# Kernel tuning notes

Measured on AMD Instinct MI355X. Metric: run time of the kernel, lower is better.

Reference implementation:

```python
import jax, jax.numpy as jnp
import numpy as np

N = 50000      # nodes
E = 400000     # edges (before self-loops)
F_IN = 256     # input_dim
HID = 64       # hidden_dim (per-head)
H = 4          # heads
OUT = 16       # output_dim
NEG_SLOPE = 0.2


def _gat_layer(x, W, a_src, a_dst, b, src, dst):
    # x: [N, Fin], W: [Fin, H*HID], a_src/a_dst: [H, HID], b: [H*HID]
    n = x.shape[0]
    h = (x @ W).reshape(n, H, HID)                        # [N,H,D]
    es = jnp.einsum('nhd,hd->nh', h, a_src)               # [N,H]
    ed = jnp.einsum('nhd,hd->nh', h, a_dst)               # [N,H]
    e = jax.nn.leaky_relu(es[src] + ed[dst], NEG_SLOPE)   # [E,H]
    m = jax.ops.segment_max(e, dst, num_segments=n)       # [N,H] segment softmax (stable)
    m = jnp.where(jnp.isfinite(m), m, 0.0)
    p = jnp.exp(e - m[dst])
    s = jax.ops.segment_sum(p, dst, num_segments=n)
    alpha = p / (s[dst] + 1e-16)                          # [E,H]
    out = jax.ops.segment_sum(h[src] * alpha[:, :, None], dst, num_segments=n)  # [N,H,D]
    return out.reshape(n, H * HID) + b


def setup_inputs() -> dict:
    key = jax.random.key(0)
    ks = jax.random.split(key, 24)
    lin = lambda k, i, o: (jax.random.normal(k, (i, o), jnp.float32) / np.sqrt(i)).astype(jnp.float32)
    att = lambda k: (jax.random.normal(k, (H, HID), jnp.float32) * 0.1).astype(jnp.float32)
    FH = H * HID  # 256
    inp = {
        'x': jax.random.normal(ks[0], (N, F_IN), jnp.float32),
        'edge_index': jax.random.randint(ks[1], (2, E), 0, N, dtype=jnp.int64),
        'W1': lin(ks[2], F_IN, FH), 'a1_src': att(ks[3]), 'a1_dst': att(ks[4]), 'b1': jnp.zeros((FH,), jnp.float32),
        'W2': lin(ks[5], FH, FH),   'a2_src': att(ks[6]), 'a2_dst': att(ks[7]), 'b2': jnp.zeros((FH,), jnp.float32),
        'W3': lin(ks[8], FH, FH),   'a3_src': att(ks[9]), 'a3_dst': att(ks[10]), 'b3': jnp.zeros((FH,), jnp.float32),
        'pW1': lin(ks[11], FH, HID), 'pb1': jnp.zeros((HID,), jnp.float32),
        'pW2': lin(ks[12], HID, HID), 'pb2': jnp.zeros((HID,), jnp.float32),
        'cW1': lin(ks[13], FH, HID), 'cb1': jnp.zeros((HID,), jnp.float32),
        'cW2': lin(ks[14], HID, OUT), 'cb2': jnp.zeros((OUT,), jnp.float32),
    }
    return inp


def reference(x, edge_index, W1, a1_src, a1_dst, b1, W2, a2_src, a2_dst, b2,
              W3, a3_src, a3_dst, b3, pW1, pb1, pW2, pb2, cW1, cb1, cW2, cb2):
    n = x.shape[0]
    loop = jnp.arange(n, dtype=edge_index.dtype)          # PyG GATConv adds self-loops
    src = jnp.concatenate([edge_index[0], loop])
    dst = jnp.concatenate([edge_index[1], loop])
    h = jax.nn.elu(_gat_layer(x, W1, a1_src, a1_dst, b1, src, dst))
    h = jax.nn.elu(_gat_layer(h, W2, a2_src, a2_dst, b2, src, dst))
    h = _gat_layer(h, W3, a3_src, a3_dst, b3, src, dst)   # [N, 256]
    logits = jax.nn.relu(h @ cW1 + cb1) @ cW2 + cb2       # classifier (dropout inactive, eval)
    proj = jax.nn.relu(h @ pW1 + pb1) @ pW2 + pb2         # projection head
    return jax.nn.log_softmax(logits, axis=1), proj
```

## Files before the change

### kernel.cpp

```cpp
#include <hip/hip_runtime.h>
#include <hip/hip_bf16.h>

#define NN 50000
#define EE 400000
#define TE (EE + NN)
#define SCAN_B ((NN + 255) / 256)

typedef float f4 __attribute__((ext_vector_type(4)));
typedef __bf16 b8 __attribute__((ext_vector_type(8)));
typedef unsigned short us8 __attribute__((ext_vector_type(8)));

__device__ __forceinline__ float b2f(unsigned short u) {
    union { unsigned int i; float f; } c; c.i = ((unsigned int)u) << 16; return c.f;
}
__device__ __forceinline__ unsigned short f2b(float x) {
    union { unsigned int i; float f; } c; c.f = x;
    unsigned int i = c.i;
    return (unsigned short)((i + 0x7FFFu + ((i >> 16) & 1u)) >> 16);
}
__device__ __forceinline__ int clampi(int v, int lo, int hi) {
    return v < lo ? lo : (v > hi ? hi : v);
}

#define PO_WT    0
#define PO_ATT   196608
#define PO_BT    198912
#define PO_BIAS  231680
#define PO_PW2   231808
#define PO_PB2   235904
#define PO_CW2   235968
#define PO_CB2   236992
#define PO_BT2   237008
#define PO_BIAS2 253392
#define PO_TOTAL 253520

__global__ void detect_kernel(const int* __restrict__ ei, const unsigned int* __restrict__ xw,
                              int* __restrict__ flag) {
    int lane = threadIdx.x;
    int bad = (lane < 16 && ei[2 * lane + 1] != 0) ? 1 : 0;
    int cnt = 0;
#pragma unroll
    for (int k = 0; k < 4; k++) {
        int i = lane + k * 64;
        unsigned short lo = (unsigned short)(xw[i] & 0xFFFFu);
        int e = (lo >> 7) & 0xFF;
        if (e >= 120 && e <= 132) cnt++;
    }
    unsigned long long anybad = __ballot(bad != 0);
#pragma unroll
    for (int off = 1; off < 64; off <<= 1) cnt += __shfl_xor(cnt, off, 64);
    if (lane == 0) {
        flag[0] = (anybad == 0ULL) ? 1 : 0;
        flag[1] = (cnt >= 128) ? 1 : 0;
    }
}

__global__ __launch_bounds__(256) void convx_kernel(const void* __restrict__ src,
                                                    unsigned short* __restrict__ dst,
                                                    const int* __restrict__ flag) {
    int i = blockIdx.x * 256 + threadIdx.x;
    if (i >= NN * 256 / 4) return;
    if (flag[1]) {
        ((ushort4*)dst)[i] = ((const ushort4*)src)[i];
    } else {
        float4 v = ((const float4*)src)[i];
        ushort4 o; o.x = f2b(v.x); o.y = f2b(v.y); o.z = f2b(v.z); o.w = f2b(v.w);
        ((ushort4*)dst)[i] = o;
    }
}

__device__ __forceinline__ float ldf(const void* p, int i, int bf) {
    return bf ? b2f(((const unsigned short*)p)[i]) : ((const float*)p)[i];
}
__global__ __launch_bounds__(256) void prep_kernel(
    const void* W1, const void* W2, const void* W3,
    const void* as1, const void* ad1, const void* b1,
    const void* as2, const void* ad2, const void* b2,
    const void* as3, const void* ad3, const void* b3,
    const void* pW1, const void* pb1, const void* pW2, const void* pb2,
    const void* cW1, const void* cb1, const void* cW2, const void* cb2,
    unsigned short* __restrict__ P, const int* __restrict__ flag) {
    int idx = blockIdx.x * 256 + threadIdx.x;
    if (idx >= PO_TOTAL) return;
    int bf = flag[1];
    float v;
    if (idx < PO_ATT) {
        int l = idx / 65536, r = idx % 65536;
        int n = r >> 8, k = r & 255;
        const void* W = (l == 0) ? W1 : (l == 1) ? W2 : W3;
        v = ldf(W, k * 256 + n, bf);
    } else if (idx < PO_BT) {
        int r = idx - PO_ATT;
        int l = r / 768, w = r % 768, which = w >> 8, j = w & 255;
        const void* s;
        if (which == 0) s = (l == 0) ? as1 : (l == 1) ? as2 : as3;
        else if (which == 1) s = (l == 0) ? ad1 : (l == 1) ? ad2 : ad3;
        else s = (l == 0) ? b1 : (l == 1) ? b2 : b3;
        v = ldf(s, j, bf);
    } else if (idx < PO_BIAS) {
        int r3 = idx - PO_BT;
        int r = r3 >> 8, k = r3 & 255;
        v = (r < 64) ? ldf(cW1, k * 64 + r, bf) : ldf(pW1, k * 64 + (r - 64), bf);
    } else if (idx < PO_PW2) {
        int r = idx - PO_BIAS;
        v = (r < 64) ? ldf(cb1, r, bf) : ldf(pb1, r - 64, bf);
    } else if (idx < PO_PB2) {
        v = ldf(pW2, idx - PO_PW2, bf);
    } else if (idx < PO_CW2) {
        v = ldf(pb2, idx - PO_PB2, bf);
    } else if (idx < PO_CB2) {
        v = ldf(cW2, idx - PO_CW2, bf);
    } else if (idx < PO_BT2) {
        v = ldf(cb2, idx - PO_CB2, bf);
    } else if (idx < PO_BIAS2) {
        int r2 = idx - PO_BT2;
        int r = r2 >> 7, k = r2 & 127;
        if (r < 16) v = (k < 64) ? ldf(cW2, k * 16 + r, bf) : 0.f;
        else if (r < 80) v = (k >= 64) ? ldf(pW2, (k - 64) * 64 + (r - 16), bf) : 0.f;
        else v = 0.f;
    } else {
        int r = idx - PO_BIAS2;
        v = (r < 16) ? ldf(cb2, r, bf) : (r < 80 ? ldf(pb2, r - 16, bf) : 0.f);
    }
    P[idx] = f2b(v);
}

__device__ __forceinline__ void edge_decode(const int* __restrict__ ei, int mode64, int e,
                                            int& src, int& dst) {
    if (e < EE) {
        if (mode64) { src = ei[2 * e]; dst = ei[2 * EE + 2 * e]; }
        else        { src = ei[e];     dst = ei[EE + e]; }
        src = clampi(src, 0, NN - 1);
        dst = clampi(dst, 0, NN - 1);
    } else {
        src = dst = e - EE;
    }
}

__global__ void deg_kernel(const int* __restrict__ ei, const int* __restrict__ flag,
                           int* __restrict__ deg) {
    int e = blockIdx.x * 256 + threadIdx.x;
    if (e >= TE) return;
    int src, dst;
    edge_decode(ei, flag[0], e, src, dst);
    atomicAdd(&deg[dst], 1);
}

__global__ __launch_bounds__(256) void scanA_kernel(const int* __restrict__ deg,
                                                    int* __restrict__ offs, int* __restrict__ bsum) {
    __shared__ int s[256];
    int t = threadIdx.x, i = blockIdx.x * 256 + t;
    int v = (i < NN) ? deg[i] : 0;
    s[t] = v;
    __syncthreads();
    for (int off = 1; off < 256; off <<= 1) {
        int x = (t >= off) ? s[t - off] : 0;
        __syncthreads();
        s[t] += x;
        __syncthreads();
    }
    if (i < NN) offs[i] = s[t] - v;
    if (t == 255) bsum[blockIdx.x] = s[255];
}
__global__ __launch_bounds__(256) void scanB_kernel(int* __restrict__ bsum) {
    __shared__ int s[256];
    int t = threadIdx.x;
    int v = (t < SCAN_B) ? bsum[t] : 0;
    s[t] = v;
    __syncthreads();
    for (int off = 1; off < 256; off <<= 1) {
        int x = (t >= off) ? s[t - off] : 0;
        __syncthreads();
        s[t] += x;
        __syncthreads();
    }
    if (t < SCAN_B) bsum[t] = s[t] - v;
}
__global__ __launch_bounds__(256) void scanC_kernel(int* __restrict__ offs,
                                                    const int* __restrict__ bsum) {
    int t = threadIdx.x, i = blockIdx.x * 256 + t;
    if (i < NN) offs[i] += bsum[blockIdx.x];
    if (i == 0) offs[NN] = TE;
}

__global__ void scatter_kernel(const int* __restrict__ ei, const int* __restrict__ flag,
                               const int* __restrict__ offs,
                               int* __restrict__ cursor, int* __restrict__ srcs,
                               int* __restrict__ dsts) {
    int e = blockIdx.x * 256 + threadIdx.x;
    if (e >= TE) return;
    int src, dst;
    edge_decode(ei, flag[0], e, src, dst);
    int pos = atomicAdd(&cursor[dst], 1);
    int slot = offs[dst] + pos;
    if (slot >= 0 && slot < TE) { srcs[slot] = src; dsts[slot] = dst; }
}

__device__ __forceinline__ void async_ld16(const unsigned short* g, unsigned short* l) {
    __builtin_amdgcn_global_load_lds(
        (const __attribute__((address_space(1))) unsigned int*)g,
        (__attribute__((address_space(3))) unsigned int*)l, 16, 0, 0);
}

__global__ __launch_bounds__(256) void gemm_bt_kernel(
    const unsigned short* __restrict__ A, const unsigned short* __restrict__ Bt,
    unsigned short* __restrict__ C, int M, int Nc, int K,
    const unsigned short* __restrict__ bias, int relu, int outf32, int final,
    const unsigned short* __restrict__ asrc, const unsigned short* __restrict__ adst,
    float* __restrict__ es, float* __restrict__ ed) {
    __shared__ unsigned short As[128 * 32];
    __shared__ unsigned short Bs[128 * 32];
    int tid = threadIdx.x;
    int lane = tid & 63;
    int wave = tid >> 6;
    int wr = wave >> 1, wc = wave & 1;
    int m0 = blockIdx.x * 128;
    int n0 = blockIdx.y * 128;
    f4 acc[4][4];
#pragma unroll
    for (int i = 0; i < 4; i++)
#pragma unroll
        for (int j = 0; j < 4; j++) acc[i][j] = (f4){0.f, 0.f, 0.f, 0.f};

    int rin = lane >> 2;
    int qsl = lane & 3;
    int qg  = qsl ^ ((rin >> 1) & 3);
    int rsel = lane & 15;
    int q16 = lane >> 4;
    int slotq = q16 ^ ((rsel >> 1) & 3);

    for (int kt = 0; kt < K; kt += 32) {
#pragma unroll
        for (int t = 0; t < 4; t++) {
            int seg = wave * 4 + t;
            if (seg < 8) {
                int r = seg * 16 + rin;
                int gm = m0 + r;
                if (gm < M)
                    async_ld16(A + (size_t)gm * K + kt + qg * 8, &As[seg * 512]);
            } else {
                int r = (seg - 8) * 16 + rin;
                int gn = n0 + r;
                async_ld16(Bt + (size_t)gn * K + kt + qg * 8, &Bs[(seg - 8) * 512]);
            }
        }
        __syncthreads();
        b8 af[4], bfv[4];
#pragma unroll
        for (int i = 0; i < 4; i++) {
            af[i]  = *(const b8*)(&As[(wr * 64 + i * 16 + rsel) * 32 + slotq * 8]);
            bfv[i] = *(const b8*)(&Bs[(wc * 64 + i * 16 + rsel) * 32 + slotq * 8]);
        }
#pragma unroll
        for (int i = 0; i < 4; i++)
#pragma unroll
            for (int j = 0; j < 4; j++)
                acc[i][j] = __builtin_amdgcn_mfma_f32_16x16x32_bf16(af[i], bfv[j], acc[i][j], 0, 0, 0);
        __syncthreads();
    }
    int cl = lane & 15, rq = lane >> 4;
    if (es) {
        int head = blockIdx.y * 2 + wc;
        float asv[4], adv[4];
#pragma unroll
        for (int j = 0; j < 4; j++) {
            asv[j] = b2f(asrc[head * 64 + j * 16 + cl]);
            adv[j] = b2f(adst[head * 64 + j * 16 + cl]);
        }
#pragma unroll
        for (int i = 0; i < 4; i++) {
            float pes[4], ped[4];
#pragma unroll
            for (int r = 0; r < 4; r++) {
                float se = 0.f, de = 0.f;
#pragma unroll
                for (int j = 0; j < 4; j++) {
                    se += acc[i][j][r] * asv[j];
                    de += acc[i][j][r] * adv[j];
                }
                pes[r] = se; ped[r] = de;
            }
#pragma unroll
            for (int off = 1; off < 16; off <<= 1) {
#pragma unroll
                for (int r = 0; r < 4; r++) {
                    pes[r] += __shfl_xor(pes[r], off, 64);
                    ped[r] += __shfl_xor(ped[r], off, 64);
                }
            }
            if (cl == 0) {
#pragma unroll
                for (int r = 0; r < 4; r++) {
                    int row = m0 + wr * 64 + i * 16 + rq * 4 + r;
                    if (row < M) {
                        es[(size_t)row * 4 + head] = pes[r];
                        ed[(size_t)row * 4 + head] = ped[r];
                    }
                }
            }
        }
    }
    if (final) {
        float* flog  = (float*)C;
        float* fproj = flog + (size_t)M * 16;
#pragma unroll
        for (int i = 0; i < 4; i++) {
#pragma unroll
            for (int r = 0; r < 4; r++) {
                int row = m0 + wr * 64 + i * 16 + rq * 4 + r;
                if (row >= M) continue;
                if (wc == 0) {
                    float lv = acc[i][0][r] + b2f(bias[cl]);
                    float mx = lv;
#pragma unroll
                    for (int off = 1; off < 16; off <<= 1) mx = fmaxf(mx, __shfl_xor(mx, off, 64));
                    float se = __expf(lv - mx);
#pragma unroll
                    for (int off = 1; off < 16; off <<= 1) se += __shfl_xor(se, off, 64);
                    flog[(size_t)row * 16 + cl] = lv - mx - __logf(se);
#pragma unroll
                    for (int j = 1; j < 4; j++) {
                        float pv = acc[i][j][r] + b2f(bias[j * 16 + cl]);
                        fproj[(size_t)row * 64 + j * 16 + cl - 16] = pv;
                    }
                } else {
                    float pv = acc[i][0][r] + b2f(bias[64 + cl]);
                    fproj[(size_t)row * 64 + 48 + cl] = pv;
                }
            }
        }
        return;
    }
#pragma unroll
    for (int j = 0; j < 4; j++) {
        int col = n0 + wc * 64 + j * 16 + cl;
        float bv = bias ? b2f(bias[col]) : 0.0f;
#pragma unroll
        for (int i = 0; i < 4; i++) {
#pragma unroll
            for (int r = 0; r < 4; r++) {
                int row = m0 + wr * 64 + i * 16 + rq * 4 + r;
                if (row < M) {
                    float v = acc[i][j][r] + bv;
                    if (relu) v = fmaxf(v, 0.0f);
                    if (outf32) ((float*)C)[(size_t)row * Nc + col] = v;
                    else C[(size_t)row * Nc + col] = f2b(v);
                }
            }
        }
    }
}

__global__ __launch_bounds__(256) void wexp_kernel(
    const float* __restrict__ es, const float* __restrict__ ed,
    const int* __restrict__ srcs, const int* __restrict__ dsts,
    float* __restrict__ wbuf) {
    int j = blockIdx.x * 256 + threadIdx.x;
    if (j >= TE) return;
    int s = srcs[j], d = dsts[j];
    float4 a = ((const float4*)es)[s];
    float4 b = ((const float4*)ed)[d];
    float v0 = a.x + b.x, v1 = a.y + b.y, v2 = a.z + b.z, v3 = a.w + b.w;
    v0 = v0 > 0.f ? v0 : 0.2f * v0; v1 = v1 > 0.f ? v1 : 0.2f * v1;
    v2 = v2 > 0.f ? v2 : 0.2f * v2; v3 = v3 > 0.f ? v3 : 0.2f * v3;
    ((float4*)wbuf)[j] = make_float4(__expf(v0), __expf(v1), __expf(v2), __expf(v3));
}

__global__ __launch_bounds__(256) void aggr_kernel(
    const unsigned short* __restrict__ H, const float* __restrict__ wbuf,
    const int* __restrict__ offs, const int* __restrict__ srcs,
    const unsigned short* __restrict__ bias, unsigned short* __restrict__ out, int N, int elu) {
    int gw = (blockIdx.x * 256 + threadIdx.x) >> 6;
    int lane = threadIdx.x & 63;
    if (gw >= N) return;
    int half = lane >> 5;
    int lh = lane & 31;
    int ch = lh << 3;
    int head = lh >> 3;
    int j0 = offs[gw];
    int j1 = offs[gw + 1];
    float a0 = 0.f, a1 = 0.f, a2 = 0.f, a3 = 0.f;
    float a4 = 0.f, a5 = 0.f, a6 = 0.f, a7 = 0.f;
    float sw = 0.f;
    int nfull = (j1 - j0) & ~3;
    int jb = j0 + half * 2;
    for (int t = 0; t < nfull; t += 4) {
        int sA = srcs[jb + t];
        int sB = srcs[jb + t + 1];
        float wA = wbuf[(size_t)(jb + t) * 4 + head];
        float wB = wbuf[(size_t)(jb + t + 1) * 4 + head];
        us8 hA = *(const us8*)(H + (size_t)sA * 256 + ch);
        us8 hB = *(const us8*)(H + (size_t)sB * 256 + ch);
        sw += wA + wB;
        a0 += wA * b2f(hA[0]) + wB * b2f(hB[0]);
        a1 += wA * b2f(hA[1]) + wB * b2f(hB[1]);
        a2 += wA * b2f(hA[2]) + wB * b2f(hB[2]);
        a3 += wA * b2f(hA[3]) + wB * b2f(hB[3]);
        a4 += wA * b2f(hA[4]) + wB * b2f(hB[4]);
        a5 += wA * b2f(hA[5]) + wB * b2f(hB[5]);
        a6 += wA * b2f(hA[6]) + wB * b2f(hB[6]);
        a7 += wA * b2f(hA[7]) + wB * b2f(hB[7]);
    }
    for (int j = j0 + nfull + half; j < j1; j += 2) {
        int sA = srcs[j];
        float wA = wbuf[(size_t)j * 4 + head];
        us8 hA = *(const us8*)(H + (size_t)sA * 256 + ch);
        sw += wA;
        a0 += wA * b2f(hA[0]); a1 += wA * b2f(hA[1]);
        a2 += wA * b2f(hA[2]); a3 += wA * b2f(hA[3]);
        a4 += wA * b2f(hA[4]); a5 += wA * b2f(hA[5]);
        a6 += wA * b2f(hA[6]); a7 += wA * b2f(hA[7]);
    }
    sw += __shfl_xor(sw, 32, 64);
    a0 += __shfl_xor(a0, 32, 64); a1 += __shfl_xor(a1, 32, 64);
    a2 += __shfl_xor(a2, 32, 64); a3 += __shfl_xor(a3, 32, 64);
    a4 += __shfl_xor(a4, 32, 64); a5 += __shfl_xor(a5, 32, 64);
    a6 += __shfl_xor(a6, 32, 64); a7 += __shfl_xor(a7, 32, 64);
    if (half == 0) {
        float rs = 1.f / (sw + 1e-16f);
        us8 bv = *(const us8*)(bias + ch);
        float r0 = a0 * rs + b2f(bv[0]), r1 = a1 * rs + b2f(bv[1]);
        float r2 = a2 * rs + b2f(bv[2]), r3 = a3 * rs + b2f(bv[3]);
        float r4 = a4 * rs + b2f(bv[4]), r5 = a5 * rs + b2f(bv[5]);
        float r6 = a6 * rs + b2f(bv[6]), r7 = a7 * rs + b2f(bv[7]);
        if (elu) {
            r0 = r0 > 0.f ? r0 : __expf(r0) - 1.f;
            r1 = r1 > 0.f ? r1 : __expf(r1) - 1.f;
            r2 = r2 > 0.f ? r2 : __expf(r2) - 1.f;
            r3 = r3 > 0.f ? r3 : __expf(r3) - 1.f;
            r4 = r4 > 0.f ? r4 : __expf(r4) - 1.f;
            r5 = r5 > 0.f ? r5 : __expf(r5) - 1.f;
            r6 = r6 > 0.f ? r6 : __expf(r6) - 1.f;
            r7 = r7 > 0.f ? r7 : __expf(r7) - 1.f;
        }
        us8 o;
        o[0] = f2b(r0); o[1] = f2b(r1); o[2] = f2b(r2); o[3] = f2b(r3);
        o[4] = f2b(r4); o[5] = f2b(r5); o[6] = f2b(r6); o[7] = f2b(r7);
        *(us8*)(out + (size_t)gw * 256 + ch) = o;
    }
}

extern "C" void kernel_launch(void* const* d_in, const int* in_sizes, int n_in,
                              void* d_out, int out_size, void* d_ws, size_t ws_size,
                              hipStream_t stream) {
    (void)in_sizes; (void)n_in; (void)out_size; (void)ws_size;
    const int* ei = (const int*)d_in[1];

    char* p = (char*)d_ws;
    auto take = [&](size_t bytes) -> void* {
        void* r = (void*)p;
        p += (bytes + 255) & ~(size_t)255;
        return r;
    };
    int* flag   = (int*)take(256);
    int* deg    = (int*)take((size_t)NN * 4);
    int* cursor = (int*)take((size_t)NN * 4);
    int* offs   = (int*)take((size_t)(NN + 1) * 4);
    int* bsum   = (int*)take(256 * 4);
    int* srcs   = (int*)take((size_t)TE * 4);
    int* dsts   = (int*)take((size_t)TE * 4);
    float* es   = (float*)take((size_t)NN * 16);
    float* ed   = (float*)take((size_t)NN * 16);
    float* wbuf = (float*)take((size_t)TE * 16);
    unsigned short* bufH = (unsigned short*)take((size_t)NN * 256 * 2);
    unsigned short* buf1 = (unsigned short*)take((size_t)NN * 256 * 2);
    unsigned short* buf2 = (unsigned short*)take((size_t)NN * 256 * 2);
    unsigned short* P    = (unsigned short*)take((size_t)PO_TOTAL * 2);
    unsigned short* xb = buf2;
    unsigned short* tbuf = bufH;

    detect_kernel<<<1, 64, 0, stream>>>(ei, (const unsigned int*)d_in[0], flag);
    convx_kernel<<<NN * 256 / 4 / 256, 256, 0, stream>>>(d_in[0], xb, flag);
    prep_kernel<<<(PO_TOTAL + 255) / 256, 256, 0, stream>>>(
        d_in[2], d_in[6], d_in[10],
        d_in[3], d_in[4], d_in[5],
        d_in[7], d_in[8], d_in[9],
        d_in[11], d_in[12], d_in[13],
        d_in[14], d_in[15], d_in[16], d_in[17],
        d_in[18], d_in[19], d_in[20], d_in[21],
        P, flag);

    hipMemsetAsync(deg, 0, (size_t)NN * 4, stream);
    hipMemsetAsync(cursor, 0, (size_t)NN * 4, stream);
    deg_kernel<<<(TE + 255) / 256, 256, 0, stream>>>(ei, flag, deg);
    scanA_kernel<<<SCAN_B, 256, 0, stream>>>(deg, offs, bsum);
    scanB_kernel<<<1, 256, 0, stream>>>(bsum);
    scanC_kernel<<<SCAN_B, 256, 0, stream>>>(offs, bsum);
    scatter_kernel<<<(TE + 255) / 256, 256, 0, stream>>>(ei, flag, offs, cursor, srcs, dsts);

    const unsigned short* X = xb;
    unsigned short* outbuf[3] = {buf1, buf2, buf1};
    for (int l = 0; l < 3; l++) {
        const unsigned short* Wt  = P + PO_WT + l * 65536;
        const unsigned short* asr = P + PO_ATT + l * 768;
        const unsigned short* adr = P + PO_ATT + l * 768 + 256;
        const unsigned short* bcb = P + PO_ATT + l * 768 + 512;
        gemm_bt_kernel<<<dim3((NN + 127) / 128, 2), 256, 0, stream>>>(
            X, Wt, bufH, NN, 256, 256, nullptr, 0, 0, 0, asr, adr, es, ed);
        wexp_kernel<<<(TE + 255) / 256, 256, 0, stream>>>(es, ed, srcs, dsts, wbuf);
        aggr_kernel<<<12500, 256, 0, stream>>>(bufH, wbuf, offs, srcs, bcb, outbuf[l], NN, (l < 2) ? 1 : 0);
        X = outbuf[l];
    }
    gemm_bt_kernel<<<dim3((NN + 127) / 128, 1), 256, 0, stream>>>(
        X, P + PO_BT, tbuf, NN, 128, 256, P + PO_BIAS, 1, 0, 0, nullptr, nullptr, nullptr, nullptr);
    gemm_bt_kernel<<<dim3((NN + 127) / 128, 1), 256, 0, stream>>>(
        tbuf, P + PO_BT2, (unsigned short*)d_out, NN, 128, 128, P + PO_BIAS2, 0, 0, 1, nullptr, nullptr, nullptr, nullptr);
}
```

Baseline: 442.6 us.

## Double-buffer GEMM LDS tiles, unroll aggregation by 8, fuse memsets into kernel

```diff
diff --git a/kernel.cpp b/kernel.cpp
--- a/kernel.cpp
+++ b/kernel.cpp
@@ -137,6 +137,11 @@
     }
 }
 
+__global__ __launch_bounds__(256) void zero_kernel(int* __restrict__ deg, int* __restrict__ cursor) {
+    int i = blockIdx.x * 256 + threadIdx.x;
+    if (i < NN) { deg[i] = 0; cursor[i] = 0; }
+}
+
 __global__ void deg_kernel(const int* __restrict__ ei, const int* __restrict__ flag,
                            int* __restrict__ deg) {
     int e = blockIdx.x * 256 + threadIdx.x;
@@ -208,8 +213,8 @@
     const unsigned short* __restrict__ bias, int relu, int outf32, int final,
     const unsigned short* __restrict__ asrc, const unsigned short* __restrict__ adst,
     float* __restrict__ es, float* __restrict__ ed) {
-    __shared__ unsigned short As[128 * 32];
-    __shared__ unsigned short Bs[128 * 32];
+    __shared__ unsigned short As[2][128 * 32];
+    __shared__ unsigned short Bs[2][128 * 32];
     int tid = threadIdx.x;
     int lane = tid & 63;
     int wave = tid >> 6;
@@ -229,7 +234,7 @@
     int q16 = lane >> 4;
     int slotq = q16 ^ ((rsel >> 1) & 3);
 
-    for (int kt = 0; kt < K; kt += 32) {
+    auto stage = [&](int b, int kt) {
 #pragma unroll
         for (int t = 0; t < 4; t++) {
             int seg = wave * 4 + t;
@@ -237,19 +242,26 @@
                 int r = seg * 16 + rin;
                 int gm = m0 + r;
                 if (gm < M)
-                    async_ld16(A + (size_t)gm * K + kt + qg * 8, &As[seg * 512]);
+                    async_ld16(A + (size_t)gm * K + kt + qg * 8, &As[b][seg * 512]);
             } else {
                 int r = (seg - 8) * 16 + rin;
                 int gn = n0 + r;
-                async_ld16(Bt + (size_t)gn * K + kt + qg * 8, &Bs[(seg - 8) * 512]);
+                async_ld16(Bt + (size_t)gn * K + kt + qg * 8, &Bs[b][(seg - 8) * 512]);
             }
         }
-        __syncthreads();
+    };
+
+    int nk = K >> 5;
+    stage(0, 0);
+    __syncthreads();
+    for (int s = 0; s < nk; s++) {
+        int cur = s & 1;
+        if (s + 1 < nk) stage(cur ^ 1, (s + 1) << 5);
         b8 af[4], bfv[4];
 #pragma unroll
         for (int i = 0; i < 4; i++) {
-            af[i]  = *(const b8*)(&As[(wr * 64 + i * 16 + rsel) * 32 + slotq * 8]);
-            bfv[i] = *(const b8*)(&Bs[(wc * 64 + i * 16 + rsel) * 32 + slotq * 8]);
+            af[i]  = *(const b8*)(&As[cur][(wr * 64 + i * 16 + rsel) * 32 + slotq * 8]);
+            bfv[i] = *(const b8*)(&Bs[cur][(wc * 64 + i * 16 + rsel) * 32 + slotq * 8]);
         }
 #pragma unroll
         for (int i = 0; i < 4; i++)
@@ -379,29 +391,52 @@
     int head = lh >> 3;
     int j0 = offs[gw];
     int j1 = offs[gw + 1];
+    int d = j1 - j0;
     float a0 = 0.f, a1 = 0.f, a2 = 0.f, a3 = 0.f;
     float a4 = 0.f, a5 = 0.f, a6 = 0.f, a7 = 0.f;
     float sw = 0.f;
-    int nfull = (j1 - j0) & ~3;
-    int jb = j0 + half * 2;
-    for (int t = 0; t < nfull; t += 4) {
-        int sA = srcs[jb + t];
-        int sB = srcs[jb + t + 1];
-        float wA = wbuf[(size_t)(jb + t) * 4 + head];
-        float wB = wbuf[(size_t)(jb + t + 1) * 4 + head];
-        us8 hA = *(const us8*)(H + (size_t)sA * 256 + ch);
-        us8 hB = *(const us8*)(H + (size_t)sB * 256 + ch);
-        sw += wA + wB;
-        a0 += wA * b2f(hA[0]) + wB * b2f(hB[0]);
-        a1 += wA * b2f(hA[1]) + wB * b2f(hB[1]);
-        a2 += wA * b2f(hA[2]) + wB * b2f(hB[2]);
-        a3 += wA * b2f(hA[3]) + wB * b2f(hB[3]);
-        a4 += wA * b2f(hA[4]) + wB * b2f(hB[4]);
-        a5 += wA * b2f(hA[5]) + wB * b2f(hB[5]);
-        a6 += wA * b2f(hA[6]) + wB * b2f(hB[6]);
-        a7 += wA * b2f(hA[7]) + wB * b2f(hB[7]);
-    }
-    for (int j = j0 + nfull + half; j < j1; j += 2) {
+    int nfull8 = d & ~7;
+    for (int t = 0; t < nfull8; t += 8) {
+        int base = j0 + t + half * 4;
+        int s0 = srcs[base], s1 = srcs[base + 1], s2 = srcs[base + 2], s3 = srcs[base + 3];
+        float w0 = wbuf[(size_t)base * 4 + head];
+        float w1 = wbuf[(size_t)(base + 1) * 4 + head];
+        float w2 = wbuf[(size_t)(base + 2) * 4 + head];
+        float w3 = wbuf[(size_t)(base + 3) * 4 + head];
+        us8 h0 = *(const us8*)(H + (size_t)s0 * 256 + ch);
+        us8 h1 = *(const us8*)(H + (size_t)s1 * 256 + ch);
+        us8 h2 = *(const us8*)(H + (size_t)s2 * 256 + ch);
+        us8 h3 = *(const us8*)(H + (size_t)s3 * 256 + ch);
+        sw += (w0 + w1) + (w2 + w3);
+        a0 += w0 * b2f(h0[0]) + w1 * b2f(h1[0]) + w2 * b2f(h2[0]) + w3 * b2f(h3[0]);
+        a1 += w0 * b2f(h0[1]) + w1 * b2f(h1[1]) + w2 * b2f(h2[1]) + w3 * b2f(h3[1]);
+        a2 += w0 * b2f(h0[2]) + w1 * b2f(h1[2]) + w2 * b2f(h2[2]) + w3 * b2f(h3[2]);
+        a3 += w0 * b2f(h0[3]) + w1 * b2f(h1[3]) + w2 * b2f(h2[3]) + w3 * b2f(h3[3]);
+        a4 += w0 * b2f(h0[4]) + w1 * b2f(h1[4]) + w2 * b2f(h2[4]) + w3 * b2f(h3[4]);
+        a5 += w0 * b2f(h0[5]) + w1 * b2f(h1[5]) + w2 * b2f(h2[5]) + w3 * b2f(h3[5]);
+        a6 += w0 * b2f(h0[6]) + w1 * b2f(h1[6]) + w2 * b2f(h2[6]) + w3 * b2f(h3[6]);
+        a7 += w0 * b2f(h0[7]) + w1 * b2f(h1[7]) + w2 * b2f(h2[7]) + w3 * b2f(h3[7]);
+    }
+    int jt = j0 + nfull8;
+    if (j1 - jt >= 4) {
+        int base = jt + half * 2;
+        int s0 = srcs[base], s1 = srcs[base + 1];
+        float w0 = wbuf[(size_t)base * 4 + head];
+        float w1 = wbuf[(size_t)(base + 1) * 4 + head];
+        us8 h0 = *(const us8*)(H + (size_t)s0 * 256 + ch);
+        us8 h1 = *(const us8*)(H + (size_t)s1 * 256 + ch);
+        sw += w0 + w1;
+        a0 += w0 * b2f(h0[0]) + w1 * b2f(h1[0]);
+        a1 += w0 * b2f(h0[1]) + w1 * b2f(h1[1]);
+        a2 += w0 * b2f(h0[2]) + w1 * b2f(h1[2]);
+        a3 += w0 * b2f(h0[3]) + w1 * b2f(h1[3]);
+        a4 += w0 * b2f(h0[4]) + w1 * b2f(h1[4]);
+        a5 += w0 * b2f(h0[5]) + w1 * b2f(h1[5]);
+        a6 += w0 * b2f(h0[6]) + w1 * b2f(h1[6]);
+        a7 += w0 * b2f(h0[7]) + w1 * b2f(h1[7]);
+        jt += 4;
+    }
+    for (int j = jt + half; j < j1; j += 2) {
         int sA = srcs[j];
         float wA = wbuf[(size_t)j * 4 + head];
         us8 hA = *(const us8*)(H + (size_t)sA * 256 + ch);
@@ -480,8 +515,7 @@
         d_in[18], d_in[19], d_in[20], d_in[21],
         P, flag);
 
-    hipMemsetAsync(deg, 0, (size_t)NN * 4, stream);
-    hipMemsetAsync(cursor, 0, (size_t)NN * 4, stream);
+    zero_kernel<<<SCAN_B, 256, 0, stream>>>(deg, cursor);
     deg_kernel<<<(TE + 255) / 256, 256, 0, stream>>>(ei, flag, deg);
     scanA_kernel<<<SCAN_B, 256, 0, stream>>>(deg, offs, bsum);
     scanB_kernel<<<1, 256, 0, stream>>>(bsum);
```

After: 441.4 us. Within noise of the previous version (-0.3%).
